# Kernel tuning notes

Measured on AMD Instinct MI355X. Metric: run time of the kernel, lower is better.

## Reference

```python
import jax, jax.numpy as jnp
import numpy as np

NUM_HEADS = 16


def rotary_pos_emb(x):
    # x: [b, h, s, d] with interleaved rotary pairs (d even)
    d, s = x.shape[-1], x.shape[-2]
    ts = jnp.arange(0, d, 2, dtype=jnp.float32)
    inv_freqs = 10000.0 ** (-ts / d)                      # [d/2]
    grid = jnp.arange(s, dtype=jnp.float32)[:, None] * inv_freqs[None, :]  # [s, d/2]
    sin = jnp.repeat(jnp.sin(grid), 2, axis=-1)           # [s, d]
    cos = jnp.repeat(jnp.cos(grid), 2, axis=-1)           # [s, d]
    x1, x2 = x[..., ::2], x[..., 1::2]
    xs = jnp.stack([-x2, x1], axis=-1).reshape(x.shape)   # rotate pairs
    return x * cos + xs * sin


def setup_inputs() -> dict:
    key = jax.random.key(0)
    ks = jax.random.split(key, 6)
    b, l, d = 2, 2048, 1024
    x = jax.random.normal(ks[0], (b, l, d), dtype=jnp.float32)
    # additive causal mask: 0 on/below diag, large negative above
    causal = jnp.tril(jnp.ones((l, l), dtype=bool))
    mask = jnp.where(causal, 0.0, -1e9).astype(jnp.float32)[None, None]  # [1,1,l,l]
    s = 0.01  # VarianceScaling(0.01)-ish small init
    Wq = jax.random.normal(ks[1], (d, d), dtype=jnp.float32) * s
    Wk = jax.random.normal(ks[2], (d, d), dtype=jnp.float32) * s
    Wv = jax.random.normal(ks[3], (d, d), dtype=jnp.float32) * s
    Wo = jax.random.normal(ks[4], (d, d), dtype=jnp.float32) * s
    return {"x": x, "mask": mask, "Wq": Wq, "Wk": Wk, "Wv": Wv, "Wo": Wo}


def reference(x, mask, Wq, Wk, Wv, Wo):
    b, l, d = x.shape
    h = NUM_HEADS
    k_sz = d // h
    split = lambda t: t.reshape(b, l, h, k_sz).transpose(0, 2, 1, 3)  # b h l k
    # NOTE: original scales q by 1/sqrt(model_dim) (not key_size), before RoPE
    q = split(x @ Wq / jnp.sqrt(jnp.float32(d)))
    q = rotary_pos_emb(q)
    k = rotary_pos_emb(split(x @ Wk))
    v = split(x @ Wv)
    logits = jnp.einsum('bhik,bhjk->bhij', q, k) + mask   # [b,h,l,l]
    a = jax.nn.softmax(logits, axis=-1)
    y = jnp.einsum('bhij,bhjv->bhiv', a, v)               # [b,h,l,k]
    y = y.transpose(0, 2, 1, 3).reshape(b, l, d)
    return y @ Wo
```

## Files before the change

kernel.cpp:

```cpp
#include <hip/hip_runtime.h>
#include <math.h>

#define L 2048
#define D 1024
#define H 16
#define KS 64
#define BBATCH 2

typedef float f32x4 __attribute__((ext_vector_type(4)));
typedef short s16x8 __attribute__((ext_vector_type(8)));

__device__ __forceinline__ ushort f2bf(float f) {
    union { float f; unsigned u; } v; v.f = f;
    unsigned lsb = (v.u >> 16) & 1u;
    v.u += 0x7fffu + lsb;
    return (ushort)(v.u >> 16);
}

__device__ __forceinline__ unsigned fbits(float f) {
    union { float f; unsigned u; } v; v.f = f; return v.u;
}

__device__ __forceinline__ void gl_lds16(const ushort* g, ushort* l) {
    __builtin_amdgcn_global_load_lds(
        (const __attribute__((address_space(1))) unsigned int*)g,
        (__attribute__((address_space(3))) unsigned int*)l, 16, 0, 0);
}

__global__ __launch_bounds__(256)
void prep(const float* __restrict__ x,
          const float* __restrict__ W0, const float* __restrict__ W1,
          const float* __restrict__ W2, const float* __restrict__ W3,
          ushort* __restrict__ xb, ushort* __restrict__ Wt,
          float2* __restrict__ tab)
{
    __shared__ float T[32][33];
    const int bid = blockIdx.x;
    const int tid = threadIdx.x;
    if (bid < 4096) {
        const int i = bid * 1024 + tid * 4;
        const float4 v = *(const float4*)&x[i];
        ushort4 p = make_ushort4(f2bf(v.x), f2bf(v.y), f2bf(v.z), f2bf(v.w));
        *(ushort4*)&xb[i] = p;
    } else if (bid < 8192) {
        const int t = bid - 4096;
        const int z = t >> 10;
        const float* W = (z == 0) ? W0 : (z == 1) ? W1 : (z == 2) ? W2 : W3;
        ushort* out = Wt + (size_t)z * D * D;
        const int r0 = ((t >> 5) & 31) * 32, c0 = (t & 31) * 32;
        const int tr = tid >> 3, tc = (tid & 7) * 4;
        const float4 v = *(const float4*)&W[(size_t)(r0 + tr) * D + c0 + tc];
        T[tr][tc + 0] = v.x; T[tr][tc + 1] = v.y;
        T[tr][tc + 2] = v.z; T[tr][tc + 3] = v.w;
        __syncthreads();
        ushort4 p = make_ushort4(f2bf(T[tc + 0][tr]), f2bf(T[tc + 1][tr]),
                                 f2bf(T[tc + 2][tr]), f2bf(T[tc + 3][tr]));
        *(ushort4*)&out[(size_t)(c0 + tr) * D + r0 + tc] = p;
    } else {
        const int idx = (bid - 8192) * 256 + tid;
        const int dd2 = idx >> 11, s = idx & 2047;
        const float inv = __expf(-(float)(2 * dd2) * (9.210340371976184f / 64.0f));
        float sn, cs;
        sincosf((float)s * inv, &sn, &cs);
        tab[idx] = make_float2(cs, sn);
    }
}

__global__ __launch_bounds__(512, 2)
void qkv_gemm(const ushort* __restrict__ A, const ushort* __restrict__ B,
              const float2* __restrict__ tab,
              ushort* __restrict__ Qo, ushort* __restrict__ Ko,
              ushort* __restrict__ Vto)
{
    __shared__ __align__(16) ushort smem[57344];
    const int tid  = threadIdx.x;
    const int wv   = tid >> 6, lane = tid & 63;
    const int i16  = lane & 15, quad = lane >> 4;
    const int wr   = wv >> 2, wc = wv & 3;

    int bid = blockIdx.y * 16 + blockIdx.x;
    bid = (bid & 7) * 32 + (bid >> 3);
    const int by = bid & 15, bx = bid >> 4;
    const int m0 = by * 192, n0 = bx * 256;

    const bool isAw = (wv < 4);
    const int cb = isAw ? tid : (tid - 256);
    const ushort* Mp = isAw ? A : B;
    const int rbase = isAw ? m0 : n0;
    const int lbo   = isAw ? 0 : 6144;
    const int c0 = cb, c1 = 256 + cb, c2 = 512 + cb, c3 = 768 + cb;
    const size_t src0 = (size_t)(rbase + (c0 >> 2)) * D + (((c0 & 3) * 8) ^ (((c0 >> 4) & 3) << 3));
    const size_t src1 = (size_t)(rbase + (c1 >> 2)) * D + (((c1 & 3) * 8) ^ (((c1 >> 4) & 3) << 3));
    const size_t src2 = (size_t)(rbase + (c2 >> 2)) * D + (((c2 & 3) * 8) ^ (((c2 >> 4) & 3) << 3));
    const size_t src3 = (size_t)(rbase + (c3 >> 2)) * D + (((c3 & 3) * 8) ^ (((c3 >> 4) & 3) << 3));
    const int ldo0 = lbo + c0 * 8, ldo1 = lbo + c1 * 8;
    const int ldo2 = lbo + c2 * 8, ldo3 = lbo + c3 * 8;

    f32x4 acc[6][4];
    #pragma unroll
    for (int i = 0; i < 6; ++i)
        #pragma unroll
        for (int j = 0; j < 4; ++j) acc[i][j] = (f32x4){0.f, 0.f, 0.f, 0.f};

#define STAGE1(kt) do { ushort* S_ = smem + ((kt) & 3) * 14336;               \
        gl_lds16(Mp + src0 + (size_t)(kt) * 32, S_ + ldo0);                   \
        gl_lds16(Mp + src1 + (size_t)(kt) * 32, S_ + ldo1); } while (0)
#define STAGE2(kt) do { ushort* S_ = smem + ((kt) & 3) * 14336;               \
        gl_lds16(Mp + src2 + (size_t)(kt) * 32, S_ + ldo2);                   \
        if (!isAw) gl_lds16(Mp + src3 + (size_t)(kt) * 32, S_ + ldo3); } while (0)

    STAGE1(0); STAGE2(0);
    STAGE1(1); STAGE2(1);
    STAGE1(2); STAGE2(2);
    if (isAw) { asm volatile("s_waitcnt vmcnt(6)" ::: "memory"); }
    else      { asm volatile("s_waitcnt vmcnt(8)" ::: "memory"); }
    __builtin_amdgcn_s_barrier();

    #pragma unroll 1
    for (int kt = 0; kt < 32; ++kt) {
        const ushort* As = smem + (kt & 3) * 14336;
        const ushort* Bs = As + 6144;
        s16x8 afr[3], bfr[4];

        #pragma unroll
        for (int mf = 0; mf < 3; ++mf) {
            int ad = (wr * 96 + mf * 16 + i16) * 64 + quad * 16;
            ad ^= ((ad >> 8) & 3) << 4;
            afr[mf] = *(const s16x8*)((const char*)As + ad);
        }
        #pragma unroll
        for (int nf = 0; nf < 4; ++nf) {
            int ad = (wc * 64 + nf * 16 + i16) * 64 + quad * 16;
            ad ^= ((ad >> 8) & 3) << 4;
            bfr[nf] = *(const s16x8*)((const char*)Bs + ad);
        }
        if (kt < 29) STAGE1(kt + 3);
        __builtin_amdgcn_s_barrier();
        asm volatile("s_waitcnt lgkmcnt(0)" ::: "memory");
        __builtin_amdgcn_sched_barrier(0);
        __builtin_amdgcn_s_setprio(1);
        #pragma unroll
        for (int mf = 0; mf < 3; ++mf)
            #pragma unroll
            for (int nf = 0; nf < 4; ++nf)
                acc[mf][nf] = __builtin_amdgcn_mfma_f32_16x16x32_bf16(
                    afr[mf], bfr[nf], acc[mf][nf], 0, 0, 0);
        __builtin_amdgcn_s_setprio(0);
        __builtin_amdgcn_s_barrier();

        #pragma unroll
        for (int mf = 0; mf < 3; ++mf) {
            int ad = (wr * 96 + (mf + 3) * 16 + i16) * 64 + quad * 16;
            ad ^= ((ad >> 8) & 3) << 4;
            afr[mf] = *(const s16x8*)((const char*)As + ad);
        }
        if (kt < 29) STAGE2(kt + 3);
        __builtin_amdgcn_s_barrier();
        asm volatile("s_waitcnt lgkmcnt(0)" ::: "memory");
        __builtin_amdgcn_sched_barrier(0);
        __builtin_amdgcn_s_setprio(1);
        #pragma unroll
        for (int mf = 0; mf < 3; ++mf)
            #pragma unroll
            for (int nf = 0; nf < 4; ++nf)
                acc[mf + 3][nf] = __builtin_amdgcn_mfma_f32_16x16x32_bf16(
                    afr[mf], bfr[nf], acc[mf + 3][nf], 0, 0, 0);
        __builtin_amdgcn_s_setprio(0);

        if (kt <= 28) {
            if (isAw) { asm volatile("s_waitcnt vmcnt(6)" ::: "memory"); }
            else      { asm volatile("s_waitcnt vmcnt(8)" ::: "memory"); }
        } else if (kt == 29) {
            if (isAw) { asm volatile("s_waitcnt vmcnt(3)" ::: "memory"); }
            else      { asm volatile("s_waitcnt vmcnt(4)" ::: "memory"); }
        } else if (kt == 30) {
            asm volatile("s_waitcnt vmcnt(0)" ::: "memory");
        }
        __builtin_amdgcn_s_barrier();
    }
#undef STAGE1
#undef STAGE2

    const int tbase = n0 + wc * 64;
    ushort* T = smem + wv * 1152;
    #pragma unroll
    for (int mf = 0; mf < 6; ++mf) {
        const int dim0 = m0 + wr * 96 + mf * 16;
        const int region = dim0 >> 10;
        if (region < 2) {
            ushort* out = (region == 0) ? Qo : Ko;
            const bool isQ = (region == 0);
            const int qd = (dim0 & 1023) + quad * 4;
            const int hh = qd >> 6, dd = qd & 63;
            #pragma unroll
            for (int nf = 0; nf < 4; ++nf) {
                const int token = tbase + nf * 16 + i16;
                const int b = token >> 11, s = token & 2047;
                ushort4 p;
                #pragma unroll
                for (int pr = 0; pr < 2; ++pr) {
                    float e = acc[mf][nf][2 * pr];
                    float o = acc[mf][nf][2 * pr + 1];
                    if (isQ) { e *= 0.03125f; o *= 0.03125f; }
                    const float2 cssn = tab[(size_t)((dd >> 1) + pr) * 2048 + s];
                    const float ne = e * cssn.x - o * cssn.y;
                    const float no = o * cssn.x + e * cssn.y;
                    if (pr == 0) { p.x = f2bf(ne); p.y = f2bf(no); }
                    else         { p.z = f2bf(ne); p.w = f2bf(no); }
                }
                *(ushort4*)&out[((size_t)(b * H + hh) * L + s) * KS + dd] = p;
            }
        } else {
            #pragma unroll
            for (int nf = 0; nf < 4; ++nf)
                #pragma unroll
                for (int r = 0; r < 4; ++r)
                    T[(quad * 4 + r) * 72 + nf * 16 + i16] = f2bf(acc[mf][nf][r]);
            __builtin_amdgcn_s_waitcnt(0);
            const int tl0 = (lane & 7) * 8;
            #pragma unroll
            for (int c = 0; c < 2; ++c) {
                const int vl = c * 8 + (lane >> 3);
                const s16x8 val = *(const s16x8*)&T[vl * 72 + tl0];
                const int vdim = (dim0 - 2048) + vl;
                const int hh = vdim >> 6, dd = vdim & 63;
                const int token0 = tbase + tl0;
                const int b = token0 >> 11, s0 = token0 & 2047;
                *(s16x8*)&Vto[((size_t)(b * H + hh) * KS + dd) * L + s0] = val;
            }
            __builtin_amdgcn_s_waitcnt(0);
        }
    }
}

__global__ __launch_bounds__(256)
void oproj_gemm(const ushort* __restrict__ A, const ushort* __restrict__ B,
                float* __restrict__ out)
{
    __shared__ __align__(16) ushort smem[32768];
    const int tid  = threadIdx.x;
    const int wv   = tid >> 6, lane = tid & 63;
    const int i16  = lane & 15, quad = lane >> 4;
    const int wr   = wv >> 1, wc = wv & 1;

    const int bid = blockIdx.y * 8 + blockIdx.x;
    const int bx  = bid & 7, by = bid >> 3;
    const int m0  = by * 128, n0 = bx * 128;

    const int c0 = tid, c1 = tid + 256;
    const size_t sA0 = (size_t)(m0 + (c0 >> 2)) * D + (((c0 & 3) * 8) ^ (((c0 >> 4) & 3) << 3));
    const size_t sA1 = (size_t)(m0 + (c1 >> 2)) * D + (((c1 & 3) * 8) ^ (((c1 >> 4) & 3) << 3));
    const size_t sB0 = (size_t)(n0 + (c0 >> 2)) * D + (((c0 & 3) * 8) ^ (((c0 >> 4) & 3) << 3));
    const size_t sB1 = (size_t)(n0 + (c1 >> 2)) * D + (((c1 & 3) * 8) ^ (((c1 >> 4) & 3) << 3));
    const int l0 = c0 * 8, l1 = c1 * 8;

    f32x4 acc[4][4];
    #pragma unroll
    for (int i = 0; i < 4; ++i)
        #pragma unroll
        for (int j = 0; j < 4; ++j) acc[i][j] = (f32x4){0.f, 0.f, 0.f, 0.f};

#define OSTAGE(kt) do { ushort* As_ = smem + ((kt) & 3) * 8192;               \
        gl_lds16(A + sA0 + (size_t)(kt) * 32, As_ + l0);                      \
        gl_lds16(A + sA1 + (size_t)(kt) * 32, As_ + l1);                      \
        gl_lds16(B + sB0 + (size_t)(kt) * 32, As_ + 4096 + l0);               \
        gl_lds16(B + sB1 + (size_t)(kt) * 32, As_ + 4096 + l1); } while (0)

    OSTAGE(0); OSTAGE(1); OSTAGE(2);
    asm volatile("s_waitcnt vmcnt(8)" ::: "memory");
    __builtin_amdgcn_s_barrier();

    #pragma unroll 1
    for (int kt = 0; kt < 32; ++kt) {
        const ushort* As = smem + (kt & 3) * 8192;
        const ushort* Bs = As + 4096;
        s16x8 afr[4], bfr[4];
        #pragma unroll
        for (int mf = 0; mf < 4; ++mf) {
            int ad = (wr * 64 + mf * 16 + i16) * 64 + quad * 16;
            ad ^= ((ad >> 8) & 3) << 4;
            afr[mf] = *(const s16x8*)((const char*)As + ad);
        }
        #pragma unroll
        for (int nf = 0; nf < 4; ++nf) {
            int ad = (wc * 64 + nf * 16 + i16) * 64 + quad * 16;
            ad ^= ((ad >> 8) & 3) << 4;
            bfr[nf] = *(const s16x8*)((const char*)Bs + ad);
        }
        if (kt < 29) OSTAGE(kt + 3);
        __builtin_amdgcn_s_barrier();
        asm volatile("s_waitcnt lgkmcnt(0)" ::: "memory");
        __builtin_amdgcn_sched_barrier(0);
        __builtin_amdgcn_s_setprio(1);
        #pragma unroll
        for (int mf = 0; mf < 4; ++mf)
            #pragma unroll
            for (int nf = 0; nf < 4; ++nf)
                acc[mf][nf] = __builtin_amdgcn_mfma_f32_16x16x32_bf16(
                    afr[mf], bfr[nf], acc[mf][nf], 0, 0, 0);
        __builtin_amdgcn_s_setprio(0);

        if (kt <= 28)      { asm volatile("s_waitcnt vmcnt(8)" ::: "memory"); }
        else if (kt == 29) { asm volatile("s_waitcnt vmcnt(4)" ::: "memory"); }
        else if (kt == 30) { asm volatile("s_waitcnt vmcnt(0)" ::: "memory"); }
        __builtin_amdgcn_s_barrier();
    }
#undef OSTAGE

    #pragma unroll
    for (int mf = 0; mf < 4; ++mf)
        #pragma unroll
        for (int nf = 0; nf < 4; ++nf) {
            const int od = n0 + wc * 64 + nf * 16 + i16;
            const int tk = m0 + wr * 64 + mf * 16 + quad * 4;
            #pragma unroll
            for (int r = 0; r < 4; ++r)
                out[(size_t)(tk + r) * D + od] = acc[mf][nf][r];
        }
}

__global__ __launch_bounds__(512)
void attn_mfma(const ushort* __restrict__ Q, const ushort* __restrict__ K,
               const ushort* __restrict__ Vt, ushort* __restrict__ Yb)
{
    const int bh   = blockIdx.y;
    const int qt   = (bh < 16) ? (15 - blockIdx.x) : blockIdx.x;
    const int tid  = threadIdx.x;
    const int wave = tid >> 6, lane = tid & 63;
    const int i16  = lane & 15, quad = lane >> 4;
    const int r0   = qt * 128 + wave * 16;
    const int row  = r0 + i16;
    const int jtmax = (r0 + 15) >> 6;
    const int jtend = 2 * qt + 1;

    __shared__ ushort Ks[2][64 * 72];
    __shared__ ushort Vs[2][64 * 72];
    __shared__ ushort Ps[8][16 * 72];

    const ushort* Qb = Q  + (size_t)bh * L * KS;
    const ushort* Kb = K  + (size_t)bh * L * KS;
    const ushort* Vb = Vt + (size_t)bh * KS * L;

    const s16x8 qf0 = *(const s16x8*)(Qb + (size_t)row * KS + quad * 8);
    const s16x8 qf1 = *(const s16x8*)(Qb + (size_t)row * KS + 32 + quad * 8);

    const int sr = tid >> 3, sseg = (tid & 7) * 8;
    s16x8 kpre = *(const s16x8*)(Kb + (size_t)sr * KS + sseg);
    s16x8 vpre = *(const s16x8*)(Vb + (size_t)sr * L + sseg);
    *(s16x8*)&Ks[0][sr * 72 + sseg] = kpre;
    *(s16x8*)&Vs[0][sr * 72 + sseg] = vpre;
    __syncthreads();

    f32x4 O0 = {0.f,0.f,0.f,0.f}, O1 = O0, O2 = O0, O3 = O0;
    float psum = 0.0f;

    for (int jt = 0; jt <= jtend; ++jt) {
        const int cur = jt & 1;
        const bool has_next = (jt < jtend);

        if (has_next) {
            const int j0n = (jt + 1) * 64;
            kpre = *(const s16x8*)(Kb + (size_t)(j0n + sr) * KS + sseg);
            vpre = *(const s16x8*)(Vb + (size_t)sr * L + j0n + sseg);
        }

        if (jt <= jtmax) {
            const int j0 = jt * 64;
            const ushort* Ksb = &Ks[cur][0];
            const ushort* Vsb = &Vs[cur][0];
            f32x4 st[4];
            #pragma unroll
            for (int nt = 0; nt < 4; ++nt) {
                const s16x8 kf0 = *(const s16x8*)&Ksb[(nt * 16 + i16) * 72 + quad * 8];
                const s16x8 kf1 = *(const s16x8*)&Ksb[(nt * 16 + i16) * 72 + 32 + quad * 8];
                f32x4 c = {0.f,0.f,0.f,0.f};
                c = __builtin_amdgcn_mfma_f32_16x16x32_bf16(kf0, qf0, c, 0, 0, 0);
                c = __builtin_amdgcn_mfma_f32_16x16x32_bf16(kf1, qf1, c, 0, 0, 0);
                st[nt] = c;
            }
            if (jt == jtmax) {
                #pragma unroll
                for (int nt = 0; nt < 4; ++nt)
                    #pragma unroll
                    for (int rg = 0; rg < 4; ++rg) {
                        const int j = j0 + nt * 16 + quad * 4 + rg;
                        if (j > row) st[nt][rg] = -1e30f;
                    }
            }
            float pv[4][4];
            #pragma unroll
            for (int nt = 0; nt < 4; ++nt)
                #pragma unroll
                for (int rg = 0; rg < 4; ++rg) {
                    pv[nt][rg] = __expf(st[nt][rg]);
                    psum += pv[nt][rg];
                }
            ushort* P2 = &Ps[wave][0];
            #pragma unroll
            for (int nt = 0; nt < 4; ++nt) {
                uint2 pk;
                pk.x = __builtin_amdgcn_perm(fbits(pv[nt][1]), fbits(pv[nt][0]), 0x07060302u);
                pk.y = __builtin_amdgcn_perm(fbits(pv[nt][3]), fbits(pv[nt][2]), 0x07060302u);
                *(uint2*)(P2 + i16 * 72 + nt * 16 + quad * 4) = pk;
            }
            const s16x8 pf0 = *(const s16x8*)(P2 + i16 * 72 + quad * 8);
            const s16x8 pf1 = *(const s16x8*)(P2 + i16 * 72 + 32 + quad * 8);
            s16x8 v0, v1;
            v0 = *(const s16x8*)&Vsb[(0 * 16 + i16) * 72 + quad * 8];
            v1 = *(const s16x8*)&Vsb[(0 * 16 + i16) * 72 + 32 + quad * 8];
            O0 = __builtin_amdgcn_mfma_f32_16x16x32_bf16(v0, pf0, O0, 0, 0, 0);
            O0 = __builtin_amdgcn_mfma_f32_16x16x32_bf16(v1, pf1, O0, 0, 0, 0);
            v0 = *(const s16x8*)&Vsb[(1 * 16 + i16) * 72 + quad * 8];
            v1 = *(const s16x8*)&Vsb[(1 * 16 + i16) * 72 + 32 + quad * 8];
            O1 = __builtin_amdgcn_mfma_f32_16x16x32_bf16(v0, pf0, O1, 0, 0, 0);
            O1 = __builtin_amdgcn_mfma_f32_16x16x32_bf16(v1, pf1, O1, 0, 0, 0);
            v0 = *(const s16x8*)&Vsb[(2 * 16 + i16) * 72 + quad * 8];
            v1 = *(const s16x8*)&Vsb[(2 * 16 + i16) * 72 + 32 + quad * 8];
            O2 = __builtin_amdgcn_mfma_f32_16x16x32_bf16(v0, pf0, O2, 0, 0, 0);
            O2 = __builtin_amdgcn_mfma_f32_16x16x32_bf16(v1, pf1, O2, 0, 0, 0);
            v0 = *(const s16x8*)&Vsb[(3 * 16 + i16) * 72 + quad * 8];
            v1 = *(const s16x8*)&Vsb[(3 * 16 + i16) * 72 + 32 + quad * 8];
            O3 = __builtin_amdgcn_mfma_f32_16x16x32_bf16(v0, pf0, O3, 0, 0, 0);
            O3 = __builtin_amdgcn_mfma_f32_16x16x32_bf16(v1, pf1, O3, 0, 0, 0);
        }

        if (has_next) {
            *(s16x8*)&Ks[cur ^ 1][sr * 72 + sseg] = kpre;
            *(s16x8*)&Vs[cur ^ 1][sr * 72 + sseg] = vpre;
            __syncthreads();
        }
    }

    psum += __shfl_xor(psum, 16);
    psum += __shfl_xor(psum, 32);
    const float inv_l = __builtin_amdgcn_rcpf(psum);
    const int b = bh >> 4, hh = bh & 15;
    ushort* Yp = Yb + ((size_t)(b * L + row)) * D + hh * KS + quad * 4;
    f32x4 r;
    r = O0 * inv_l; *(ushort4*)(Yp +  0) = make_ushort4(f2bf(r[0]),f2bf(r[1]),f2bf(r[2]),f2bf(r[3]));
    r = O1 * inv_l; *(ushort4*)(Yp + 16) = make_ushort4(f2bf(r[0]),f2bf(r[1]),f2bf(r[2]),f2bf(r[3]));
    r = O2 * inv_l; *(ushort4*)(Yp + 32) = make_ushort4(f2bf(r[0]),f2bf(r[1]),f2bf(r[2]),f2bf(r[3]));
    r = O3 * inv_l; *(ushort4*)(Yp + 48) = make_ushort4(f2bf(r[0]),f2bf(r[1]),f2bf(r[2]),f2bf(r[3]));
}

extern "C" void kernel_launch(void* const* d_in, const int* in_sizes, int n_in,
                              void* d_out, int out_size, void* d_ws, size_t ws_size,
                              hipStream_t stream)
{
    const float* x  = (const float*)d_in[0];
    const float* Wq = (const float*)d_in[2];
    const float* Wk = (const float*)d_in[3];
    const float* Wv = (const float*)d_in[4];
    const float* Wo = (const float*)d_in[5];

    const size_t NTOK = (size_t)BBATCH * L;
    const size_t SZ   = NTOK * D;
    ushort* xb  = (ushort*)d_ws;
    ushort* Wt  = xb + SZ;
    ushort* Qb  = Wt + 4 * (size_t)D * D;
    ushort* Kb  = Qb + SZ;
    ushort* Vtb = Kb + SZ;
    ushort* Yb  = Vtb + SZ;
    float2* tab = (float2*)Yb;

    prep<<<dim3(8448), dim3(256), 0, stream>>>(x, Wq, Wk, Wv, Wo, xb, Wt, tab);

    qkv_gemm<<<dim3(16, 16), dim3(512), 0, stream>>>(Wt, xb, tab, Qb, Kb, Vtb);

    attn_mfma<<<dim3(16, 32), dim3(512), 0, stream>>>(Qb, Kb, Vtb, Yb);

    oproj_gemm<<<dim3(8, 32), dim3(256), 0, stream>>>(Yb, Wt + 3 * (size_t)D * D,
                                                      (float*)d_out);
}
```

Baseline: 189.4 us.

## Give each attention wave two query row-blocks and XOR-swizzle K/V shared tiles

The attention kernel drops from 8 to 4 waves per block, and each wave now handles 32 query rows as two 16-row fragments. Each K and V fragment read from shared memory is reused across both row groups, which halves LDS traffic per MFMA. The padded 72-stride K/V tiles are replaced with unpadded 64-wide tiles that use an XOR swizzle to avoid bank conflicts. The cost is more accumulator registers per wave (launch bounds 256, 3) and a coarser causal-skip granularity per wave.

```diff
diff --git a/kernel.cpp b/kernel.cpp
--- a/kernel.cpp
+++ b/kernel.cpp
@@ -319,7 +319,7 @@
         }
 }
 
-__global__ __launch_bounds__(512)
+__global__ __launch_bounds__(256, 3)
 void attn_mfma(const ushort* __restrict__ Q, const ushort* __restrict__ K,
                const ushort* __restrict__ Vt, ushort* __restrict__ Yb)
 {
@@ -328,31 +328,49 @@
     const int tid  = threadIdx.x;
     const int wave = tid >> 6, lane = tid & 63;
     const int i16  = lane & 15, quad = lane >> 4;
-    const int r0   = qt * 128 + wave * 16;
-    const int row  = r0 + i16;
-    const int jtmax = (r0 + 15) >> 6;
+    const int r0   = qt * 128 + wave * 32;
+    const int rowa = r0 + i16;
+    const int rowb = r0 + 16 + i16;
+    const int jtmax = r0 >> 6;
     const int jtend = 2 * qt + 1;
 
-    __shared__ ushort Ks[2][64 * 72];
-    __shared__ ushort Vs[2][64 * 72];
-    __shared__ ushort Ps[8][16 * 72];
+    __shared__ __align__(16) ushort Ks[2][64 * 64];
+    __shared__ __align__(16) ushort Vs[2][64 * 64];
+    __shared__ __align__(16) ushort Ps[4][2 * 16 * 72];
 
     const ushort* Qb = Q  + (size_t)bh * L * KS;
     const ushort* Kb = K  + (size_t)bh * L * KS;
     const ushort* Vb = Vt + (size_t)bh * KS * L;
 
-    const s16x8 qf0 = *(const s16x8*)(Qb + (size_t)row * KS + quad * 8);
-    const s16x8 qf1 = *(const s16x8*)(Qb + (size_t)row * KS + 32 + quad * 8);
-
-    const int sr = tid >> 3, sseg = (tid & 7) * 8;
-    s16x8 kpre = *(const s16x8*)(Kb + (size_t)sr * KS + sseg);
-    s16x8 vpre = *(const s16x8*)(Vb + (size_t)sr * L + sseg);
-    *(s16x8*)&Ks[0][sr * 72 + sseg] = kpre;
-    *(s16x8*)&Vs[0][sr * 72 + sseg] = vpre;
+    const s16x8 qa0 = *(const s16x8*)(Qb + (size_t)rowa * KS + quad * 8);
+    const s16x8 qa1 = *(const s16x8*)(Qb + (size_t)rowa * KS + 32 + quad * 8);
+    const s16x8 qb0 = *(const s16x8*)(Qb + (size_t)rowb * KS + quad * 8);
+    const s16x8 qb1 = *(const s16x8*)(Qb + (size_t)rowb * KS + 32 + quad * 8);
+
+    const int sr  = tid >> 2;
+    const int scb = (tid & 3) * 32;
+    const int ssu = scb >> 1;
+    const int wk  = (sr & 7) << 4;
+    const int w0  = (sr * 128 + scb) ^ wk;
+    const int w1  = (sr * 128 + scb + 16) ^ wk;
+
+    s16x8 kp0 = *(const s16x8*)(Kb + (size_t)sr * KS + ssu);
+    s16x8 kp1 = *(const s16x8*)(Kb + (size_t)sr * KS + ssu + 8);
+    s16x8 vp0 = *(const s16x8*)(Vb + (size_t)sr * L + ssu);
+    s16x8 vp1 = *(const s16x8*)(Vb + (size_t)sr * L + ssu + 8);
+    *(s16x8*)((char*)&Ks[0][0] + w0) = kp0;
+    *(s16x8*)((char*)&Ks[0][0] + w1) = kp1;
+    *(s16x8*)((char*)&Vs[0][0] + w0) = vp0;
+    *(s16x8*)((char*)&Vs[0][0] + w1) = vp1;
     __syncthreads();
 
-    f32x4 O0 = {0.f,0.f,0.f,0.f}, O1 = O0, O2 = O0, O3 = O0;
-    float psum = 0.0f;
+    f32x4 Oa0 = {0.f,0.f,0.f,0.f}, Oa1 = Oa0, Oa2 = Oa0, Oa3 = Oa0;
+    f32x4 Ob0 = Oa0, Ob1 = Oa0, Ob2 = Oa0, Ob3 = Oa0;
+    float psa = 0.f, psb = 0.f;
+
+    const int xk = (i16 & 7) << 4;
+    ushort* P2a = &Ps[wave][0];
+    ushort* P2b = &Ps[wave][16 * 72];
 
     for (int jt = 0; jt <= jtend; ++jt) {
         const int cur = jt & 1;
@@ -360,87 +378,113 @@
 
         if (has_next) {
             const int j0n = (jt + 1) * 64;
-            kpre = *(const s16x8*)(Kb + (size_t)(j0n + sr) * KS + sseg);
-            vpre = *(const s16x8*)(Vb + (size_t)sr * L + j0n + sseg);
+            kp0 = *(const s16x8*)(Kb + (size_t)(j0n + sr) * KS + ssu);
+            kp1 = *(const s16x8*)(Kb + (size_t)(j0n + sr) * KS + ssu + 8);
+            vp0 = *(const s16x8*)(Vb + (size_t)sr * L + j0n + ssu);
+            vp1 = *(const s16x8*)(Vb + (size_t)sr * L + j0n + ssu + 8);
         }
 
         if (jt <= jtmax) {
             const int j0 = jt * 64;
-            const ushort* Ksb = &Ks[cur][0];
-            const ushort* Vsb = &Vs[cur][0];
-            f32x4 st[4];
+            const char* Ksb = (const char*)&Ks[cur][0];
+            const char* Vsb = (const char*)&Vs[cur][0];
+
             #pragma unroll
             for (int nt = 0; nt < 4; ++nt) {
-                const s16x8 kf0 = *(const s16x8*)&Ksb[(nt * 16 + i16) * 72 + quad * 8];
-                const s16x8 kf1 = *(const s16x8*)&Ksb[(nt * 16 + i16) * 72 + 32 + quad * 8];
-                f32x4 c = {0.f,0.f,0.f,0.f};
-                c = __builtin_amdgcn_mfma_f32_16x16x32_bf16(kf0, qf0, c, 0, 0, 0);
-                c = __builtin_amdgcn_mfma_f32_16x16x32_bf16(kf1, qf1, c, 0, 0, 0);
-                st[nt] = c;
-            }
-            if (jt == jtmax) {
-                #pragma unroll
-                for (int nt = 0; nt < 4; ++nt)
+                const int rb = (nt * 16 + i16) * 128 + quad * 16;
+                const s16x8 kf0 = *(const s16x8*)(Ksb + (rb ^ xk));
+                const s16x8 kf1 = *(const s16x8*)(Ksb + ((rb + 64) ^ xk));
+                f32x4 ca = {0.f,0.f,0.f,0.f};
+                ca = __builtin_amdgcn_mfma_f32_16x16x32_bf16(kf0, qa0, ca, 0, 0, 0);
+                ca = __builtin_amdgcn_mfma_f32_16x16x32_bf16(kf1, qa1, ca, 0, 0, 0);
+                f32x4 cb = {0.f,0.f,0.f,0.f};
+                cb = __builtin_amdgcn_mfma_f32_16x16x32_bf16(kf0, qb0, cb, 0, 0, 0);
+                cb = __builtin_amdgcn_mfma_f32_16x16x32_bf16(kf1, qb1, cb, 0, 0, 0);
+                if (jt == jtmax) {
                     #pragma unroll
                     for (int rg = 0; rg < 4; ++rg) {
                         const int j = j0 + nt * 16 + quad * 4 + rg;
-                        if (j > row) st[nt][rg] = -1e30f;
+                        if (j > rowa) ca[rg] = -1e30f;
+                        if (j > rowb) cb[rg] = -1e30f;
                     }
-            }
-            float pv[4][4];
-            #pragma unroll
-            for (int nt = 0; nt < 4; ++nt)
+                }
+                float pa[4], pb[4];
                 #pragma unroll
                 for (int rg = 0; rg < 4; ++rg) {
-                    pv[nt][rg] = __expf(st[nt][rg]);
-                    psum += pv[nt][rg];
+                    pa[rg] = __expf(ca[rg]); psa += pa[rg];
+                    pb[rg] = __expf(cb[rg]); psb += pb[rg];
                 }
-            ushort* P2 = &Ps[wave][0];
-            #pragma unroll
-            for (int nt = 0; nt < 4; ++nt) {
-                uint2 pk;
-                pk.x = __builtin_amdgcn_perm(fbits(pv[nt][1]), fbits(pv[nt][0]), 0x07060302u);
-                pk.y = __builtin_amdgcn_perm(fbits(pv[nt][3]), fbits(pv[nt][2]), 0x07060302u);
-                *(uint2*)(P2 + i16 * 72 + nt * 16 + quad * 4) = pk;
+                uint2 pka, pkb;
+                pka.x = __builtin_amdgcn_perm(fbits(pa[1]), fbits(pa[0]), 0x07060302u);
+                pka.y = __builtin_amdgcn_perm(fbits(pa[3]), fbits(pa[2]), 0x07060302u);
+                pkb.x = __builtin_amdgcn_perm(fbits(pb[1]), fbits(pb[0]), 0x07060302u);
+                pkb.y = __builtin_amdgcn_perm(fbits(pb[3]), fbits(pb[2]), 0x07060302u);
+                *(uint2*)(P2a + i16 * 72 + nt * 16 + quad * 4) = pka;
+                *(uint2*)(P2b + i16 * 72 + nt * 16 + quad * 4) = pkb;
             }
-            const s16x8 pf0 = *(const s16x8*)(P2 + i16 * 72 + quad * 8);
-            const s16x8 pf1 = *(const s16x8*)(P2 + i16 * 72 + 32 + quad * 8);
+
+            const s16x8 pa0 = *(const s16x8*)(P2a + i16 * 72 + quad * 8);
+            const s16x8 pa1 = *(const s16x8*)(P2a + i16 * 72 + 32 + quad * 8);
+            const s16x8 pb0 = *(const s16x8*)(P2b + i16 * 72 + quad * 8);
+            const s16x8 pb1 = *(const s16x8*)(P2b + i16 * 72 + 32 + quad * 8);
             s16x8 v0, v1;
-            v0 = *(const s16x8*)&Vsb[(0 * 16 + i16) * 72 + quad * 8];
-            v1 = *(const s16x8*)&Vsb[(0 * 16 + i16) * 72 + 32 + quad * 8];
-            O0 = __builtin_amdgcn_mfma_f32_16x16x32_bf16(v0, pf0, O0, 0, 0, 0);
-            O0 = __builtin_amdgcn_mfma_f32_16x16x32_bf16(v1, pf1, O0, 0, 0, 0);
-            v0 = *(const s16x8*)&Vsb[(1 * 16 + i16) * 72 + quad * 8];
-            v1 = *(const s16x8*)&Vsb[(1 * 16 + i16) * 72 + 32 + quad * 8];
-            O1 = __builtin_amdgcn_mfma_f32_16x16x32_bf16(v0, pf0, O1, 0, 0, 0);
-            O1 = __builtin_amdgcn_mfma_f32_16x16x32_bf16(v1, pf1, O1, 0, 0, 0);
-            v0 = *(const s16x8*)&Vsb[(2 * 16 + i16) * 72 + quad * 8];
-            v1 = *(const s16x8*)&Vsb[(2 * 16 + i16) * 72 + 32 + quad * 8];
-            O2 = __builtin_amdgcn_mfma_f32_16x16x32_bf16(v0, pf0, O2, 0, 0, 0);
-            O2 = __builtin_amdgcn_mfma_f32_16x16x32_bf16(v1, pf1, O2, 0, 0, 0);
-            v0 = *(const s16x8*)&Vsb[(3 * 16 + i16) * 72 + quad * 8];
-            v1 = *(const s16x8*)&Vsb[(3 * 16 + i16) * 72 + 32 + quad * 8];
-            O3 = __builtin_amdgcn_mfma_f32_16x16x32_bf16(v0, pf0, O3, 0, 0, 0);
-            O3 = __builtin_amdgcn_mfma_f32_16x16x32_bf16(v1, pf1, O3, 0, 0, 0);
+            int vb0 = (0 * 16 + i16) * 128 + quad * 16;
+            v0 = *(const s16x8*)(Vsb + (vb0 ^ xk));
+            v1 = *(const s16x8*)(Vsb + ((vb0 + 64) ^ xk));
+            Oa0 = __builtin_amdgcn_mfma_f32_16x16x32_bf16(v0, pa0, Oa0, 0, 0, 0);
+            Oa0 = __builtin_amdgcn_mfma_f32_16x16x32_bf16(v1, pa1, Oa0, 0, 0, 0);
+            Ob0 = __builtin_amdgcn_mfma_f32_16x16x32_bf16(v0, pb0, Ob0, 0, 0, 0);
+            Ob0 = __builtin_amdgcn_mfma_f32_16x16x32_bf16(v1, pb1, Ob0, 0, 0, 0);
+            vb0 = (1 * 16 + i16) * 128 + quad * 16;
+            v0 = *(const s16x8*)(Vsb + (vb0 ^ xk));
+            v1 = *(const s16x8*)(Vsb + ((vb0 + 64) ^ xk));
+            Oa1 = __builtin_amdgcn_mfma_f32_16x16x32_bf16(v0, pa0, Oa1, 0, 0, 0);
+            Oa1 = __builtin_amdgcn_mfma_f32_16x16x32_bf16(v1, pa1, Oa1, 0, 0, 0);
+            Ob1 = __builtin_amdgcn_mfma_f32_16x16x32_bf16(v0, pb0, Ob1, 0, 0, 0);
+            Ob1 = __builtin_amdgcn_mfma_f32_16x16x32_bf16(v1, pb1, Ob1, 0, 0, 0);
+            vb0 = (2 * 16 + i16) * 128 + quad * 16;
+            v0 = *(const s16x8*)(Vsb + (vb0 ^ xk));
+            v1 = *(const s16x8*)(Vsb + ((vb0 + 64) ^ xk));
+            Oa2 = __builtin_amdgcn_mfma_f32_16x16x32_bf16(v0, pa0, Oa2, 0, 0, 0);
+            Oa2 = __builtin_amdgcn_mfma_f32_16x16x32_bf16(v1, pa1, Oa2, 0, 0, 0);
+            Ob2 = __builtin_amdgcn_mfma_f32_16x16x32_bf16(v0, pb0, Ob2, 0, 0, 0);
+            Ob2 = __builtin_amdgcn_mfma_f32_16x16x32_bf16(v1, pb1, Ob2, 0, 0, 0);
+            vb0 = (3 * 16 + i16) * 128 + quad * 16;
+            v0 = *(const s16x8*)(Vsb + (vb0 ^ xk));
+            v1 = *(const s16x8*)(Vsb + ((vb0 + 64) ^ xk));
+            Oa3 = __builtin_amdgcn_mfma_f32_16x16x32_bf16(v0, pa0, Oa3, 0, 0, 0);
+            Oa3 = __builtin_amdgcn_mfma_f32_16x16x32_bf16(v1, pa1, Oa3, 0, 0, 0);
+            Ob3 = __builtin_amdgcn_mfma_f32_16x16x32_bf16(v0, pb0, Ob3, 0, 0, 0);
+            Ob3 = __builtin_amdgcn_mfma_f32_16x16x32_bf16(v1, pb1, Ob3, 0, 0, 0);
         }
 
         if (has_next) {
-            *(s16x8*)&Ks[cur ^ 1][sr * 72 + sseg] = kpre;
-            *(s16x8*)&Vs[cur ^ 1][sr * 72 + sseg] = vpre;
+            *(s16x8*)((char*)&Ks[cur ^ 1][0] + w0) = kp0;
+            *(s16x8*)((char*)&Ks[cur ^ 1][0] + w1) = kp1;
+            *(s16x8*)((char*)&Vs[cur ^ 1][0] + w0) = vp0;
+            *(s16x8*)((char*)&Vs[cur ^ 1][0] + w1) = vp1;
             __syncthreads();
         }
     }
 
-    psum += __shfl_xor(psum, 16);
-    psum += __shfl_xor(psum, 32);
-    const float inv_l = __builtin_amdgcn_rcpf(psum);
+    psa += __shfl_xor(psa, 16);
+    psa += __shfl_xor(psa, 32);
+    psb += __shfl_xor(psb, 16);
+    psb += __shfl_xor(psb, 32);
+    const float ia = __builtin_amdgcn_rcpf(psa);
+    const float ib = __builtin_amdgcn_rcpf(psb);
     const int b = bh >> 4, hh = bh & 15;
-    ushort* Yp = Yb + ((size_t)(b * L + row)) * D + hh * KS + quad * 4;
+    ushort* Ya = Yb + ((size_t)(b * L + rowa)) * D + hh * KS + quad * 4;
+    ushort* Yc = Yb + ((size_t)(b * L + rowb)) * D + hh * KS + quad * 4;
     f32x4 r;
-    r = O0 * inv_l; *(ushort4*)(Yp +  0) = make_ushort4(f2bf(r[0]),f2bf(r[1]),f2bf(r[2]),f2bf(r[3]));
-    r = O1 * inv_l; *(ushort4*)(Yp + 16) = make_ushort4(f2bf(r[0]),f2bf(r[1]),f2bf(r[2]),f2bf(r[3]));
-    r = O2 * inv_l; *(ushort4*)(Yp + 32) = make_ushort4(f2bf(r[0]),f2bf(r[1]),f2bf(r[2]),f2bf(r[3]));
-    r = O3 * inv_l; *(ushort4*)(Yp + 48) = make_ushort4(f2bf(r[0]),f2bf(r[1]),f2bf(r[2]),f2bf(r[3]));
+    r = Oa0 * ia; *(ushort4*)(Ya +  0) = make_ushort4(f2bf(r[0]),f2bf(r[1]),f2bf(r[2]),f2bf(r[3]));
+    r = Oa1 * ia; *(ushort4*)(Ya + 16) = make_ushort4(f2bf(r[0]),f2bf(r[1]),f2bf(r[2]),f2bf(r[3]));
+    r = Oa2 * ia; *(ushort4*)(Ya + 32) = make_ushort4(f2bf(r[0]),f2bf(r[1]),f2bf(r[2]),f2bf(r[3]));
+    r = Oa3 * ia; *(ushort4*)(Ya + 48) = make_ushort4(f2bf(r[0]),f2bf(r[1]),f2bf(r[2]),f2bf(r[3]));
+    r = Ob0 * ib; *(ushort4*)(Yc +  0) = make_ushort4(f2bf(r[0]),f2bf(r[1]),f2bf(r[2]),f2bf(r[3]));
+    r = Ob1 * ib; *(ushort4*)(Yc + 16) = make_ushort4(f2bf(r[0]),f2bf(r[1]),f2bf(r[2]),f2bf(r[3]));
+    r = Ob2 * ib; *(ushort4*)(Yc + 32) = make_ushort4(f2bf(r[0]),f2bf(r[1]),f2bf(r[2]),f2bf(r[3]));
+    r = Ob3 * ib; *(ushort4*)(Yc + 48) = make_ushort4(f2bf(r[0]),f2bf(r[1]),f2bf(r[2]),f2bf(r[3]));
 }
 
 extern "C" void kernel_launch(void* const* d_in, const int* in_sizes, int n_in,
@@ -467,7 +511,7 @@
 
     qkv_gemm<<<dim3(16, 16), dim3(512), 0, stream>>>(Wt, xb, tab, Qb, Kb, Vtb);
 
-    attn_mfma<<<dim3(16, 32), dim3(512), 0, stream>>>(Qb, Kb, Vtb, Yb);
+    attn_mfma<<<dim3(16, 32), dim3(256), 0, stream>>>(Qb, Kb, Vtb, Yb);
 
     oproj_gemm<<<dim3(8, 32), dim3(256), 0, stream>>>(Yb, Wt + 3 * (size_t)D * D,
                                                       (float*)d_out);
```

Result: slower. 193.9 us (+2.4%).

## Stream K/V tiles via direct global-to-LDS loads with XOR-swizzled layout

Applied to the files above, without the earlier changes.

Replaces the register-staged K/V prefetch into padded shared memory with global_load_lds direct copies into an unpadded 64x64 tile. An XOR swizzle on 16-byte chunks keeps the MFMA fragment reads free of bank conflicts. This is meant to save VGPRs and the extra LDS store instructions, and to shrink LDS footprint. The cost is a full vmcnt(0) wait before each barrier, and correctness now depends on the swizzle being consistent between the load and read sides.

```diff
diff --git a/kernel.cpp b/kernel.cpp
--- a/kernel.cpp
+++ b/kernel.cpp
@@ -333,9 +333,9 @@
     const int jtmax = (r0 + 15) >> 6;
     const int jtend = 2 * qt + 1;
 
-    __shared__ ushort Ks[2][64 * 72];
-    __shared__ ushort Vs[2][64 * 72];
-    __shared__ ushort Ps[8][16 * 72];
+    __shared__ __align__(16) ushort Ks[2][64 * 64];
+    __shared__ __align__(16) ushort Vs[2][64 * 64];
+    __shared__ __align__(16) ushort Ps[8][16 * 72];
 
     const ushort* Qb = Q  + (size_t)bh * L * KS;
     const ushort* Kb = K  + (size_t)bh * L * KS;
@@ -344,35 +344,43 @@
     const s16x8 qf0 = *(const s16x8*)(Qb + (size_t)row * KS + quad * 8);
     const s16x8 qf1 = *(const s16x8*)(Qb + (size_t)row * KS + 32 + quad * 8);
 
-    const int sr = tid >> 3, sseg = (tid & 7) * 8;
-    s16x8 kpre = *(const s16x8*)(Kb + (size_t)sr * KS + sseg);
-    s16x8 vpre = *(const s16x8*)(Vb + (size_t)sr * L + sseg);
-    *(s16x8*)&Ks[0][sr * 72 + sseg] = kpre;
-    *(s16x8*)&Vs[0][sr * 72 + sseg] = vpre;
-    __syncthreads();
+    const int srow = tid >> 3;
+    const int scol = ((tid & 7) ^ ((tid >> 3) & 7)) * 8;
+    ushort* kd0 = &Ks[0][0] + tid * 8;
+    ushort* vd0 = &Vs[0][0] + tid * 8;
+    ushort* kd1 = &Ks[1][0] + tid * 8;
+    ushort* vd1 = &Vs[1][0] + tid * 8;
+
+    gl_lds16(Kb + (size_t)srow * KS + scol, kd0);
+    gl_lds16(Vb + (size_t)srow * L + scol, vd0);
+    asm volatile("s_waitcnt vmcnt(0)" ::: "memory");
+    __builtin_amdgcn_s_barrier();
 
     f32x4 O0 = {0.f,0.f,0.f,0.f}, O1 = O0, O2 = O0, O3 = O0;
     float psum = 0.0f;
-
+    const int xk = (i16 & 7) << 4;
+
+    #pragma unroll 1
     for (int jt = 0; jt <= jtend; ++jt) {
         const int cur = jt & 1;
         const bool has_next = (jt < jtend);
 
         if (has_next) {
             const int j0n = (jt + 1) * 64;
-            kpre = *(const s16x8*)(Kb + (size_t)(j0n + sr) * KS + sseg);
-            vpre = *(const s16x8*)(Vb + (size_t)sr * L + j0n + sseg);
+            gl_lds16(Kb + (size_t)(j0n + srow) * KS + scol, cur ? kd0 : kd1);
+            gl_lds16(Vb + (size_t)srow * L + j0n + scol,    cur ? vd0 : vd1);
         }
 
         if (jt <= jtmax) {
             const int j0 = jt * 64;
-            const ushort* Ksb = &Ks[cur][0];
-            const ushort* Vsb = &Vs[cur][0];
+            const char* Ksb = (const char*)&Ks[cur][0];
+            const char* Vsb = (const char*)&Vs[cur][0];
             f32x4 st[4];
             #pragma unroll
             for (int nt = 0; nt < 4; ++nt) {
-                const s16x8 kf0 = *(const s16x8*)&Ksb[(nt * 16 + i16) * 72 + quad * 8];
-                const s16x8 kf1 = *(const s16x8*)&Ksb[(nt * 16 + i16) * 72 + 32 + quad * 8];
+                const int rb = (nt * 16 + i16) * 128 + quad * 16;
+                const s16x8 kf0 = *(const s16x8*)(Ksb + (rb ^ xk));
+                const s16x8 kf1 = *(const s16x8*)(Ksb + ((rb + 64) ^ xk));
                 f32x4 c = {0.f,0.f,0.f,0.f};
                 c = __builtin_amdgcn_mfma_f32_16x16x32_bf16(kf0, qf0, c, 0, 0, 0);
                 c = __builtin_amdgcn_mfma_f32_16x16x32_bf16(kf1, qf1, c, 0, 0, 0);
@@ -406,28 +414,31 @@
             const s16x8 pf0 = *(const s16x8*)(P2 + i16 * 72 + quad * 8);
             const s16x8 pf1 = *(const s16x8*)(P2 + i16 * 72 + 32 + quad * 8);
             s16x8 v0, v1;
-            v0 = *(const s16x8*)&Vsb[(0 * 16 + i16) * 72 + quad * 8];
-            v1 = *(const s16x8*)&Vsb[(0 * 16 + i16) * 72 + 32 + quad * 8];
+            int vb0 = (0 * 16 + i16) * 128 + quad * 16;
+            v0 = *(const s16x8*)(Vsb + (vb0 ^ xk));
+            v1 = *(const s16x8*)(Vsb + ((vb0 + 64) ^ xk));
             O0 = __builtin_amdgcn_mfma_f32_16x16x32_bf16(v0, pf0, O0, 0, 0, 0);
             O0 = __builtin_amdgcn_mfma_f32_16x16x32_bf16(v1, pf1, O0, 0, 0, 0);
-            v0 = *(const s16x8*)&Vsb[(1 * 16 + i16) * 72 + quad * 8];
-            v1 = *(const s16x8*)&Vsb[(1 * 16 + i16) * 72 + 32 + quad * 8];
+            vb0 = (1 * 16 + i16) * 128 + quad * 16;
+            v0 = *(const s16x8*)(Vsb + (vb0 ^ xk));
+            v1 = *(const s16x8*)(Vsb + ((vb0 + 64) ^ xk));
             O1 = __builtin_amdgcn_mfma_f32_16x16x32_bf16(v0, pf0, O1, 0, 0, 0);
             O1 = __builtin_amdgcn_mfma_f32_16x16x32_bf16(v1, pf1, O1, 0, 0, 0);
-            v0 = *(const s16x8*)&Vsb[(2 * 16 + i16) * 72 + quad * 8];
-            v1 = *(const s16x8*)&Vsb[(2 * 16 + i16) * 72 + 32 + quad * 8];
+            vb0 = (2 * 16 + i16) * 128 + quad * 16;
+            v0 = *(const s16x8*)(Vsb + (vb0 ^ xk));
+            v1 = *(const s16x8*)(Vsb + ((vb0 + 64) ^ xk));
             O2 = __builtin_amdgcn_mfma_f32_16x16x32_bf16(v0, pf0, O2, 0, 0, 0);
             O2 = __builtin_amdgcn_mfma_f32_16x16x32_bf16(v1, pf1, O2, 0, 0, 0);
-            v0 = *(const s16x8*)&Vsb[(3 * 16 + i16) * 72 + quad * 8];
-            v1 = *(const s16x8*)&Vsb[(3 * 16 + i16) * 72 + 32 + quad * 8];
+            vb0 = (3 * 16 + i16) * 128 + quad * 16;
+            v0 = *(const s16x8*)(Vsb + (vb0 ^ xk));
+            v1 = *(const s16x8*)(Vsb + ((vb0 + 64) ^ xk));
             O3 = __builtin_amdgcn_mfma_f32_16x16x32_bf16(v0, pf0, O3, 0, 0, 0);
             O3 = __builtin_amdgcn_mfma_f32_16x16x32_bf16(v1, pf1, O3, 0, 0, 0);
         }
 
         if (has_next) {
-            *(s16x8*)&Ks[cur ^ 1][sr * 72 + sseg] = kpre;
-            *(s16x8*)&Vs[cur ^ 1][sr * 72 + sseg] = vpre;
-            __syncthreads();
+            asm volatile("s_waitcnt vmcnt(0)" ::: "memory");
+            __builtin_amdgcn_s_barrier();
         }
     }
 
```

After: 180.9 us. 1.05x faster.
